# Performance work log

Measured on AMD Instinct MI355X. Metric: run time of the kernel, lower is better.

Reference implementation:

```python
import jax, jax.numpy as jnp
import numpy as np
import math

H = 32          # num_heads
D = 128         # head_dim
HID = 2048      # hidden_size
INNER = H * D   # hidden_inner_size
BLOCK = 256
NUM_LAYERS = 32
LAYER_IDX = 0


def build_slopes(n):
    def p2(m):
        start = 2 ** (-(2 ** (-(math.log2(m) - 3))))
        return [start * (start ** i) for i in range(m)]
    if math.log2(n).is_integer():
        s = p2(n)
    else:
        c = 2 ** math.floor(math.log2(n))
        s = p2(c) + p2(2 * c)[0::2][: n - c]
    s = np.asarray(s, dtype=np.float32)
    s = s * (1.0 - LAYER_IDX / (NUM_LAYERS - 1) + 1e-5)
    return jnp.asarray(s)  # [H]


def lightning_attention(q, k, v, slope, kv0, block):
    # q,k,v: [h,n,d]; slope: [h]; kv0: [h,d,e]
    h, n, d = q.shape
    nb = n // block
    arr = jnp.arange(1, block + 1, dtype=jnp.float32)            # [m]
    s = slope[:, None, None]                                      # [h,1,1]
    q_decay = jnp.exp(-s * arr[None, :, None])                    # [h,m,1]
    k_decay = jnp.exp(-s * (block - arr)[None, :, None])          # [h,m,1]
    idx = arr[:, None] - arr[None, :]                             # [m,m]
    diag_decay = jnp.where(idx >= 0, jnp.exp(-s * idx), 0.0)      # [h,m,m]
    blk_decay = jnp.exp(-slope * block)[:, None, None]            # [h,1,1]

    qb = q.reshape(h, nb, block, d).transpose(1, 0, 2, 3)         # [nb,h,m,d]
    kb = k.reshape(h, nb, block, d).transpose(1, 0, 2, 3)
    vb = v.reshape(h, nb, block, d).transpose(1, 0, 2, 3)

    def step(kv, blk):
        qi, ki, vi = blk
        inter = jnp.einsum('hmd,hde->hme', qi * q_decay, kv)
        qk = jnp.einsum('hmd,hnd->hmn', qi, ki) * diag_decay
        intra = jnp.einsum('hmn,hne->hme', qk, vi)
        kv_new = blk_decay * kv + jnp.einsum('hmd,hme->hde', ki * k_decay, vi)
        return kv_new, inter + intra

    kv_final, out = jax.lax.scan(step, kv0, (qb, kb, vb))
    out = out.transpose(1, 0, 2, 3).reshape(h, n, d)
    return out, kv_final


def rmsnorm(x, w, eps=1e-5):
    xf = x.astype(jnp.float32)
    var = jnp.mean(xf * xf, axis=-1, keepdims=True)
    return (xf * jax.lax.rsqrt(var + eps)).astype(x.dtype) * w


def setup_inputs() -> dict:
    key = jax.random.key(0)
    ks = jax.random.split(key, 4)
    n = 4096
    return {
        'hidden_states': jax.random.normal(ks[0], (n, HID), dtype=jnp.float32),
        'positions': jnp.arange(n, dtype=jnp.int64) if jax.config.jax_enable_x64 else jnp.arange(n, dtype=jnp.int32),
        'kv_cache': jnp.zeros((H, D, D), dtype=jnp.float32),
        'W_qkv': jax.random.normal(ks[1], (HID, 3 * INNER), dtype=jnp.float32) / np.sqrt(HID),
        'W_gate': jax.random.normal(ks[2], (HID, INNER), dtype=jnp.float32) / np.sqrt(HID),
        'W_out': jax.random.normal(ks[3], (INNER, HID), dtype=jnp.float32) / np.sqrt(INNER),
        'norm_weight': jnp.ones((INNER,), dtype=jnp.float32),
    }


def reference(hidden_states, positions, kv_cache, W_qkv, W_gate, W_out, norm_weight):
    n = hidden_states.shape[0]
    slope = build_slopes(H)
    qkv = hidden_states @ W_qkv                                # [n, 3*INNER]
    act = jax.nn.silu(qkv.astype(jnp.float32)).reshape(n, H, 3 * D)
    q, k, v = jnp.split(act, 3, axis=-1)                       # [n,H,D] each
    q = q.transpose(1, 0, 2)                                   # [H,n,D]
    k = k.transpose(1, 0, 2)
    v = v.transpose(1, 0, 2)
    attn, kv_final = lightning_attention(q, k, v, slope, kv_cache.astype(jnp.float32), BLOCK)
    hidden = attn.transpose(1, 0, 2).reshape(n, INNER)          # n (h d)
    hidden = rmsnorm(hidden, norm_weight)
    gate = hidden_states @ W_gate
    hidden = jax.nn.sigmoid(gate) * hidden
    out = hidden @ W_out                                        # [n, HID]
    return out
```

## Files before the change

kernel.cpp:

```cpp
#include <hip/hip_runtime.h>
#include <hip/hip_bf16.h>
#include <cstdint>
#include <cstddef>

#define SEQ    4096
#define HEADS  32
#define HD     128
#define HIDDEN 2048
#define NINNER 4096
#define BLK    256
#define NB     16

typedef __attribute__((ext_vector_type(8))) __bf16 bf16x8;
typedef __attribute__((ext_vector_type(4))) __bf16 bf16x4;
typedef __attribute__((ext_vector_type(4))) float  f32x4;

#define MFMA16(a,b,c) __builtin_amdgcn_mfma_f32_16x16x32_bf16((a),(b),(c),0,0,0)

typedef __attribute__((address_space(1))) const unsigned int gu32;
typedef __attribute__((address_space(3))) unsigned int lu32;

__device__ __forceinline__ void gld16(void* lds, const void* g){
    __builtin_amdgcn_global_load_lds((gu32*)g, (lu32*)lds, 16, 0, 0);
}

__device__ __forceinline__ float slope_for_head(int h){
    return exp2f(-0.25f*(float)(h+1)) * 1.00001f;
}

__global__ __launch_bounds__(256)
void cast_f32_bf16(const float* __restrict__ in, __bf16* __restrict__ out, int n){
    int i = (blockIdx.x*256 + threadIdx.x)*4;
    if (i >= n) return;
    float4 v = *(const float4*)(in + i);
    bf16x4 o;
    o[0] = (__bf16)v.x; o[1] = (__bf16)v.y; o[2] = (__bf16)v.z; o[3] = (__bf16)v.w;
    *(bf16x4*)(out + i) = o;
}

__global__ __launch_bounds__(256)
void transpose_cast(const float* __restrict__ W, __bf16* __restrict__ Wt, int K, int N){
    __shared__ __align__(16) __bf16 t[64][72];
    const int tid = threadIdx.x;
    const int n0 = blockIdx.x*64, k0 = blockIdx.y*64;
    const int r = tid >> 4, c4 = tid & 15;
    #pragma unroll
    for (int i = 0; i < 4; i++){
        int k = r + i*16;
        float4 v = *(const float4*)(W + (size_t)(k0 + k)*N + n0 + c4*4);
        t[c4*4+0][k] = (__bf16)v.x;
        t[c4*4+1][k] = (__bf16)v.y;
        t[c4*4+2][k] = (__bf16)v.z;
        t[c4*4+3][k] = (__bf16)v.w;
    }
    __syncthreads();
    #pragma unroll
    for (int j = 0; j < 2; j++){
        int idx = tid + j*256;
        int n = idx >> 3, c8 = idx & 7;
        bf16x8 val = *(const bf16x8*)&t[n][c8*8];
        *(bf16x8*)(Wt + (size_t)(n0 + n)*K + k0 + c8*8) = val;
    }
}

template<int EPI>
__global__ __launch_bounds__(256,2)
void gemm_bt(const __bf16* __restrict__ A, const __bf16* __restrict__ Bt,
             float* __restrict__ Cf, __bf16* __restrict__ Cb, __bf16* __restrict__ Cb2,
             int M, int N, int K)
{
    __shared__ __align__(16) __bf16 a_lds[128*64];
    __shared__ __align__(16) __bf16 b_lds[128*64];
    const int tid  = threadIdx.x;
    const int lane = tid & 63;
    const int w    = tid >> 6;
    const int lr   = lane & 15;
    const int quad = lane >> 4;
    const int bn = blockIdx.x, bm = blockIdx.y;
    const int wm = w & 1, wn = w >> 1;

    f32x4 acc[4][4];
    #pragma unroll
    for (int i = 0; i < 4; i++)
        #pragma unroll
        for (int j = 0; j < 4; j++) acc[i][j] = (f32x4){0.f,0.f,0.f,0.f};

    const int r8 = lane >> 3;
    const int qs = (lane & 7) ^ r8;
    const __bf16* Abase = A  + (size_t)bm*128*K;
    const __bf16* Bbase = Bt + (size_t)bn*128*K;

    const int sw = lr & 7;

    for (int kb = 0; kb < K; kb += 64){
        #pragma unroll
        for (int t = 0; t < 4; t++){
            int ch = t*4 + w;
            gld16(a_lds + ch*512, Abase + (size_t)(ch*8 + r8)*K + kb + qs*8);
            gld16(b_lds + ch*512, Bbase + (size_t)(ch*8 + r8)*K + kb + qs*8);
        }
        __syncthreads();
        #pragma unroll
        for (int kk = 0; kk < 2; kk++){
            bf16x8 af[4];
            #pragma unroll
            for (int mt = 0; mt < 4; mt++)
                af[mt] = *(const bf16x8*)&a_lds[(wm*64 + mt*16 + lr)*64 + (((kk*4+quad) ^ sw)*8)];
            #pragma unroll
            for (int nt = 0; nt < 4; nt++){
                bf16x8 bfv = *(const bf16x8*)&b_lds[(wn*64 + nt*16 + lr)*64 + (((kk*4+quad) ^ sw)*8)];
                #pragma unroll
                for (int mt = 0; mt < 4; mt++)
                    acc[mt][nt] = MFMA16(af[mt], bfv, acc[mt][nt]);
            }
        }
        __syncthreads();
    }

    if constexpr (EPI == 0){
        if (bn < 96){
            const int h = bn / 3, which = bn % 3;
            __bf16* outp = Cb + (size_t)(which*HEADS + h)*SEQ*HD;
            #pragma unroll
            for (int mt = 0; mt < 4; mt++)
            #pragma unroll
            for (int nt = 0; nt < 4; nt++)
            #pragma unroll
            for (int r = 0; r < 4; r++){
                int row = bm*128 + wm*64 + mt*16 + quad*4 + r;
                int col = wn*64 + nt*16 + lr;
                float x = acc[mt][nt][r];
                float sv = x / (1.f + __expf(-x));
                outp[(size_t)row*HD + col] = (__bf16)sv;
            }
        } else {
            const int col0 = (bn - 96)*128;
            #pragma unroll
            for (int mt = 0; mt < 4; mt++)
            #pragma unroll
            for (int nt = 0; nt < 4; nt++)
            #pragma unroll
            for (int r = 0; r < 4; r++){
                int row = bm*128 + wm*64 + mt*16 + quad*4 + r;
                int col = col0 + wn*64 + nt*16 + lr;
                float x = acc[mt][nt][r];
                Cb2[(size_t)row*NINNER + col] = (__bf16)(1.f/(1.f + __expf(-x)));
            }
        }
    } else {
        #pragma unroll
        for (int mt = 0; mt < 4; mt++)
        #pragma unroll
        for (int nt = 0; nt < 4; nt++)
        #pragma unroll
        for (int r = 0; r < 4; r++){
            int row = bm*128 + wm*64 + mt*16 + quad*4 + r;
            int col = bn*128 + wn*64 + nt*16 + lr;
            Cf[(size_t)row*N + col] = acc[mt][nt][r];
        }
    }
}

__global__ __launch_bounds__(256)
void prep_T(const __bf16* __restrict__ kbuf, const __bf16* __restrict__ vbuf,
            __bf16* __restrict__ kT, __bf16* __restrict__ vT)
{
    __shared__ __align__(16) __bf16 t[128][136];
    const int tid = threadIdx.x;
    const int pb = blockIdx.x, h = blockIdx.y;
    const float s = slope_for_head(h);
    const int locbase = (pb & 1)*128;
    for (int pass = 0; pass < 2; pass++){
        const __bf16* src = pass ? vbuf : kbuf;
        __bf16* dst = pass ? vT : kT;
        __syncthreads();
        #pragma unroll
        for (int i = 0; i < 8; i++){
            int idx = tid + i*256;
            int row = idx >> 4, c = idx & 15;
            bf16x8 val = *(const bf16x8*)(src + (size_t)(h*SEQ + pb*128 + row)*HD + c*8);
            if (pass == 0){
                float dec = __expf(-s*(float)(255 - (locbase + row)));
                #pragma unroll
                for (int j = 0; j < 8; j++) val[j] = (__bf16)((float)val[j]*dec);
            }
            #pragma unroll
            for (int j = 0; j < 8; j++) t[c*8 + j][row] = val[j];
        }
        __syncthreads();
        #pragma unroll
        for (int i = 0; i < 8; i++){
            int idx = tid + i*256;
            int d = idx >> 4, c = idx & 15;
            bf16x8 val = *(const bf16x8*)&t[d][c*8];
            *(bf16x8*)(dst + (size_t)(h*HD + d)*SEQ + pb*128 + c*8) = val;
        }
    }
}

__global__ __launch_bounds__(256,2)
void pass_a(const __bf16* __restrict__ vT, const __bf16* __restrict__ kT,
            float* __restrict__ kvbT)
{
    __shared__ __align__(16) __bf16 a_lds[128*64];
    __shared__ __align__(16) __bf16 b_lds[128*64];
    const int b = blockIdx.x, h = blockIdx.y;
    const int tid = threadIdx.x, lane = tid & 63, w = tid >> 6;
    const int lr = lane & 15, quad = lane >> 4;
    const int wm = w & 1, wn = w >> 1;

    f32x4 acc[4][4];
    #pragma unroll
    for (int i = 0; i < 4; i++)
        #pragma unroll
        for (int j = 0; j < 4; j++) acc[i][j] = (f32x4){0.f,0.f,0.f,0.f};

    const int r8 = lane >> 3;
    const int qs = (lane & 7) ^ r8;
    const int sw = lr & 7;
    const __bf16* Abase = vT + (size_t)h*HD*SEQ + (size_t)b*BLK;
    const __bf16* Bbase = kT + (size_t)h*HD*SEQ + (size_t)b*BLK;

    for (int kb = 0; kb < BLK; kb += 64){
        #pragma unroll
        for (int t = 0; t < 4; t++){
            int ch = t*4 + w;
            gld16(a_lds + ch*512, Abase + (size_t)(ch*8 + r8)*SEQ + kb + qs*8);
            gld16(b_lds + ch*512, Bbase + (size_t)(ch*8 + r8)*SEQ + kb + qs*8);
        }
        __syncthreads();
        #pragma unroll
        for (int kk = 0; kk < 2; kk++){
            bf16x8 af[4];
            #pragma unroll
            for (int mt = 0; mt < 4; mt++)
                af[mt] = *(const bf16x8*)&a_lds[(wm*64 + mt*16 + lr)*64 + (((kk*4+quad) ^ sw)*8)];
            #pragma unroll
            for (int nt = 0; nt < 4; nt++){
                bf16x8 bfv = *(const bf16x8*)&b_lds[(wn*64 + nt*16 + lr)*64 + (((kk*4+quad) ^ sw)*8)];
                #pragma unroll
                for (int mt = 0; mt < 4; mt++)
                    acc[mt][nt] = MFMA16(af[mt], bfv, acc[mt][nt]);
            }
        }
        __syncthreads();
    }
    float* outp = kvbT + (size_t)(h*NB + b)*HD*HD;
    #pragma unroll
    for (int mt = 0; mt < 4; mt++)
    #pragma unroll
    for (int nt = 0; nt < 4; nt++)
    #pragma unroll
    for (int r = 0; r < 4; r++){
        int row = wm*64 + mt*16 + quad*4 + r;
        int col = wn*64 + nt*16 + lr;
        outp[(size_t)row*HD + col] = acc[mt][nt][r];
    }
}

__global__ __launch_bounds__(256)
void scan_kv(const float* __restrict__ kvbT, const float* __restrict__ kv0,
             __bf16* __restrict__ kvsT)
{
    const int chunk = blockIdx.x;
    const int h = blockIdx.y;
    const int t = threadIdx.x;
    const float s = slope_for_head(h);
    const float lam = __expf(-s*(float)BLK);
    const int le0 = chunk*2048;
    float st[8];
    #pragma unroll
    for (int j = 0; j < 8; j++){
        int le = le0 + t + 256*j;
        int e = le >> 7, d = le & 127;
        st[j] = kv0[(size_t)h*HD*HD + (size_t)d*HD + e];
    }
    for (int b = 0; b < NB; b++){
        size_t base = (size_t)(h*NB + b)*HD*HD + le0;
        #pragma unroll
        for (int j = 0; j < 8; j++) kvsT[base + t + 256*j] = (__bf16)st[j];
        #pragma unroll
        for (int j = 0; j < 8; j++) st[j] = lam*st[j] + kvbT[base + t + 256*j];
    }
}

__global__ __launch_bounds__(256,2)
void pass_c(const __bf16* __restrict__ qbuf, const __bf16* __restrict__ kbuf,
            const __bf16* __restrict__ vT, const __bf16* __restrict__ kvsT,
            float* __restrict__ attn)
{
    __shared__ __align__(16) __bf16 p_lds[4][32*72];
    const int rb = blockIdx.x & 1, b = blockIdx.x >> 1, h = blockIdx.y;
    const float s = slope_for_head(h);
    const int tid = threadIdx.x, lane = tid & 63, w = tid >> 6;
    const int lr = lane & 15, quad = lane >> 4;
    const int R0 = rb*128 + w*32;

    const __bf16* qh  = qbuf + (size_t)h*SEQ*HD + (size_t)b*BLK*HD;
    const __bf16* kh  = kbuf + (size_t)h*SEQ*HD + (size_t)b*BLK*HD;
    const __bf16* vh  = vT   + (size_t)h*HD*SEQ + (size_t)b*BLK;
    const __bf16* kvh = kvsT + (size_t)(h*NB + b)*HD*HD;

    f32x4 acc[2][8];
    #pragma unroll
    for (int i = 0; i < 2; i++)
        #pragma unroll
        for (int j = 0; j < 8; j++) acc[i][j] = (f32x4){0.f,0.f,0.f,0.f};

    bf16x8 qf[4][2];
    #pragma unroll
    for (int ks = 0; ks < 4; ks++)
        #pragma unroll
        for (int mt = 0; mt < 2; mt++)
            qf[ks][mt] = *(const bf16x8*)(qh + (size_t)(R0 + mt*16 + lr)*HD + ks*32 + quad*8);

    float qdec[2];
    #pragma unroll
    for (int mt = 0; mt < 2; mt++)
        qdec[mt] = __expf(-s*(float)(R0 + mt*16 + lr + 1));
    #pragma unroll
    for (int ks = 0; ks < 4; ks++){
        bf16x8 saf[2];
        #pragma unroll
        for (int mt = 0; mt < 2; mt++)
            #pragma unroll
            for (int j = 0; j < 8; j++) saf[mt][j] = (__bf16)((float)qf[ks][mt][j]*qdec[mt]);
        #pragma unroll
        for (int nt = 0; nt < 8; nt++){
            bf16x8 bv = *(const bf16x8*)(kvh + (size_t)(nt*16 + lr)*HD + ks*32 + quad*8);
            #pragma unroll
            for (int mt = 0; mt < 2; mt++) acc[mt][nt] = MFMA16(saf[mt], bv, acc[mt][nt]);
        }
    }

    float colf[4];
    #pragma unroll
    for (int nt = 0; nt < 4; nt++)
        colf[nt] = __expf(-s*(float)(63 - nt*16 - lr));
    const int cmax = (R0 + 31) >> 6;
    for (int c = 0; c <= cmax; c++){
        f32x4 qk[2][4];
        #pragma unroll
        for (int i = 0; i < 2; i++)
            #pragma unroll
            for (int j = 0; j < 4; j++) qk[i][j] = (f32x4){0.f,0.f,0.f,0.f};
        #pragma unroll
        for (int ks = 0; ks < 4; ks++){
            #pragma unroll
            for (int nt = 0; nt < 4; nt++){
                bf16x8 kf = *(const bf16x8*)(kh + (size_t)(c*64 + nt*16 + lr)*HD + ks*32 + quad*8);
                #pragma unroll
                for (int mt = 0; mt < 2; mt++) qk[mt][nt] = MFMA16(qf[ks][mt], kf, qk[mt][nt]);
            }
        }
        float rowf[2][4];
        #pragma unroll
        for (int mt = 0; mt < 2; mt++)
            #pragma unroll
            for (int r = 0; r < 4; r++)
                rowf[mt][r] = __expf(-s*(float)(R0 + mt*16 + quad*4 + r - c*64 - 63));
        #pragma unroll
        for (int mt = 0; mt < 2; mt++)
        #pragma unroll
        for (int nt = 0; nt < 4; nt++)
        #pragma unroll
        for (int r = 0; r < 4; r++){
            int i  = R0 + mt*16 + quad*4 + r;
            int jj = c*64 + nt*16 + lr;
            float dv = (i >= jj) ? rowf[mt][r]*colf[nt] : 0.f;
            p_lds[w][(mt*16 + quad*4 + r)*72 + nt*16 + lr] = (__bf16)(qk[mt][nt][r]*dv);
        }
        #pragma unroll
        for (int ks2 = 0; ks2 < 2; ks2++){
            bf16x8 pf[2];
            #pragma unroll
            for (int mt = 0; mt < 2; mt++)
                pf[mt] = *(const bf16x8*)&p_lds[w][(mt*16 + lr)*72 + ks2*32 + quad*8];
            #pragma unroll
            for (int nt = 0; nt < 8; nt++){
                bf16x8 vf = *(const bf16x8*)(vh + (size_t)(nt*16 + lr)*SEQ + c*64 + ks2*32 + quad*8);
                #pragma unroll
                for (int mt = 0; mt < 2; mt++) acc[mt][nt] = MFMA16(pf[mt], vf, acc[mt][nt]);
            }
        }
    }

    #pragma unroll
    for (int mt = 0; mt < 2; mt++)
    #pragma unroll
    for (int nt = 0; nt < 8; nt++)
    #pragma unroll
    for (int r = 0; r < 4; r++){
        int pos = b*BLK + R0 + mt*16 + quad*4 + r;
        int e = nt*16 + lr;
        attn[(size_t)pos*NINNER + h*HD + e] = acc[mt][nt][r];
    }
}

__global__ __launch_bounds__(256)
void rmsgate(const float* __restrict__ attn, const __bf16* __restrict__ sg,
             const float* __restrict__ nw, __bf16* __restrict__ h2)
{
    const int row = blockIdx.x, tid = threadIdx.x;
    const float* x = attn + (size_t)row*NINNER;
    float4 xs[4];
    float ss = 0.f;
    #pragma unroll
    for (int i = 0; i < 4; i++){
        xs[i] = *(const float4*)(x + (i*256 + tid)*4);
        ss += xs[i].x*xs[i].x + xs[i].y*xs[i].y + xs[i].z*xs[i].z + xs[i].w*xs[i].w;
    }
    #pragma unroll
    for (int o = 32; o > 0; o >>= 1) ss += __shfl_down(ss, o, 64);
    __shared__ float red[4];
    const int lane = tid & 63, w = tid >> 6;
    if (lane == 0) red[w] = ss;
    __syncthreads();
    float tot = red[0] + red[1] + red[2] + red[3];
    float rs = rsqrtf(tot*(1.f/NINNER) + 1e-5f);
    #pragma unroll
    for (int i = 0; i < 4; i++){
        int idx = (i*256 + tid)*4;
        float4 wv = *(const float4*)(nw + idx);
        bf16x4 sv = *(const bf16x4*)(sg + (size_t)row*NINNER + idx);
        bf16x4 o;
        o[0] = (__bf16)((float)sv[0] * xs[i].x*rs*wv.x);
        o[1] = (__bf16)((float)sv[1] * xs[i].y*rs*wv.y);
        o[2] = (__bf16)((float)sv[2] * xs[i].z*rs*wv.z);
        o[3] = (__bf16)((float)sv[3] * xs[i].w*rs*wv.w);
        *(bf16x4*)(h2 + (size_t)row*NINNER + idx) = o;
    }
}

extern "C" void kernel_launch(void* const* d_in, const int* in_sizes, int n_in,
                              void* d_out, int out_size, void* d_ws, size_t ws_size,
                              hipStream_t stream) {
    (void)in_sizes; (void)n_in; (void)out_size; (void)ws_size;
    const float* hs    = (const float*)d_in[0];
    const float* kv0   = (const float*)d_in[2];
    const float* Wqkv  = (const float*)d_in[3];
    const float* Wgate = (const float*)d_in[4];
    const float* Wout  = (const float*)d_in[5];
    const float* nw    = (const float*)d_in[6];
    float* out = (float*)d_out;

    char* ws = (char*)d_ws;
    __bf16* WqkvT  = (__bf16*)(ws);
    __bf16* WgateT = (__bf16*)(ws + 50331648);
    float*  attn   = (float*)(ws);
    __bf16* WoutT  = (__bf16*)(ws + 67108864);
    __bf16* hsb    = (__bf16*)(ws + 83886080);
    __bf16* qkvb   = (__bf16*)(ws + 100663296);
    __bf16* qbuf   = qkvb;
    __bf16* kbuf   = qkvb + (size_t)HEADS*SEQ*HD;
    __bf16* vbuf   = qkvb + (size_t)2*HEADS*SEQ*HD;
    __bf16* h2     = qkvb;
    __bf16* kT     = (__bf16*)(ws + 201326592);
    __bf16* vT     = (__bf16*)(ws + 234881024);
    float*  kvbT   = (float*) (ws + 268435456);
    __bf16* kvsT   = (__bf16*)(ws + 301989888);
    __bf16* sgate  = (__bf16*)(ws + 318767104);

    cast_f32_bf16<<<8192, 256, 0, stream>>>(hs, hsb, SEQ*HIDDEN);
    transpose_cast<<<dim3(192, 32), 256, 0, stream>>>(Wqkv,  WqkvT,  2048, 12288);
    transpose_cast<<<dim3( 64, 32), 256, 0, stream>>>(Wgate, WgateT, 2048,  4096);
    transpose_cast<<<dim3( 32, 64), 256, 0, stream>>>(Wout,  WoutT,  4096,  2048);

    gemm_bt<0><<<dim3(128, 32), 256, 0, stream>>>(hsb, WqkvT, nullptr, qkvb, sgate, 4096, 16384, 2048);

    prep_T<<<dim3(32, 32), 256, 0, stream>>>(kbuf, vbuf, kT, vT);
    pass_a<<<dim3(16, 32), 256, 0, stream>>>(vT, kT, kvbT);
    scan_kv<<<dim3(8, 32), 256, 0, stream>>>(kvbT, kv0, kvsT);
    pass_c<<<dim3(NB*2, 32), 256, 0, stream>>>(qbuf, kbuf, vT, kvsT, attn);

    rmsgate<<<4096, 256, 0, stream>>>(attn, sgate, nw, h2);
    gemm_bt<2><<<dim3(16, 32), 256, 0, stream>>>(h2, WoutT, out, nullptr, nullptr, 4096, 2048, 4096);
}
```

Before: 776.0 us.

## Fuse prep kernels, switch GEMMs to 32x32 MFMA, fold transposes into QKV epilogue

```diff
diff --git a/kernel.cpp b/kernel.cpp
--- a/kernel.cpp
+++ b/kernel.cpp
@@ -11,11 +11,13 @@
 #define BLK    256
 #define NB     16
 
-typedef __attribute__((ext_vector_type(8))) __bf16 bf16x8;
-typedef __attribute__((ext_vector_type(4))) __bf16 bf16x4;
-typedef __attribute__((ext_vector_type(4))) float  f32x4;
+typedef __attribute__((ext_vector_type(8)))  __bf16 bf16x8;
+typedef __attribute__((ext_vector_type(4)))  __bf16 bf16x4;
+typedef __attribute__((ext_vector_type(4)))  float  f32x4;
+typedef __attribute__((ext_vector_type(16))) float  f32x16;
 
 #define MFMA16(a,b,c) __builtin_amdgcn_mfma_f32_16x16x32_bf16((a),(b),(c),0,0,0)
+#define MFMA32(a,b,c) __builtin_amdgcn_mfma_f32_32x32x16_bf16((a),(b),(c),0,0,0)
 
 typedef __attribute__((address_space(1))) const unsigned int gu32;
 typedef __attribute__((address_space(3))) unsigned int lu32;
@@ -28,21 +30,9 @@
     return exp2f(-0.25f*(float)(h+1)) * 1.00001f;
 }
 
-__global__ __launch_bounds__(256)
-void cast_f32_bf16(const float* __restrict__ in, __bf16* __restrict__ out, int n){
-    int i = (blockIdx.x*256 + threadIdx.x)*4;
-    if (i >= n) return;
-    float4 v = *(const float4*)(in + i);
-    bf16x4 o;
-    o[0] = (__bf16)v.x; o[1] = (__bf16)v.y; o[2] = (__bf16)v.z; o[3] = (__bf16)v.w;
-    *(bf16x4*)(out + i) = o;
-}
-
-__global__ __launch_bounds__(256)
-void transpose_cast(const float* __restrict__ W, __bf16* __restrict__ Wt, int K, int N){
-    __shared__ __align__(16) __bf16 t[64][72];
-    const int tid = threadIdx.x;
-    const int n0 = blockIdx.x*64, k0 = blockIdx.y*64;
+__device__ __forceinline__ void tcast_block(const float* __restrict__ W, __bf16* __restrict__ Wt,
+                                            int K, int N, int bx, int by, __bf16 (*t)[72], int tid){
+    const int n0 = bx*64, k0 = by*64;
     const int r = tid >> 4, c4 = tid & 15;
     #pragma unroll
     for (int i = 0; i < 4; i++){
@@ -63,34 +53,74 @@
     }
 }
 
+__global__ __launch_bounds__(256)
+void prep_all(const float* __restrict__ hs, __bf16* __restrict__ hsb,
+              const float* __restrict__ Wqkv, __bf16* __restrict__ WqkvT,
+              const float* __restrict__ Wgate, __bf16* __restrict__ WgateT,
+              const float* __restrict__ Wout, __bf16* __restrict__ WoutT)
+{
+    __shared__ __align__(16) __bf16 t[64][72];
+    const int tid = threadIdx.x;
+    int id = blockIdx.x;
+    if (id < 8192){
+        int i = (id*256 + tid)*4;
+        float4 v = *(const float4*)(hs + i);
+        bf16x4 o;
+        o[0] = (__bf16)v.x; o[1] = (__bf16)v.y; o[2] = (__bf16)v.z; o[3] = (__bf16)v.w;
+        *(bf16x4*)(hsb + i) = o;
+    } else if (id < 14336){
+        int j = id - 8192;
+        tcast_block(Wqkv, WqkvT, 2048, 12288, j % 192, j / 192, t, tid);
+    } else if (id < 16384){
+        int j = id - 14336;
+        tcast_block(Wgate, WgateT, 2048, 4096, j % 64, j / 64, t, tid);
+    } else {
+        int j = id - 16384;
+        tcast_block(Wout, WoutT, 4096, 2048, j % 32, j / 32, t, tid);
+    }
+}
+
 template<int EPI>
 __global__ __launch_bounds__(256,2)
-void gemm_bt(const __bf16* __restrict__ A, const __bf16* __restrict__ Bt,
-             float* __restrict__ Cf, __bf16* __restrict__ Cb, __bf16* __restrict__ Cb2,
-             int M, int N, int K)
+void gemm32(const __bf16* __restrict__ A, const __bf16* __restrict__ Bt,
+            float* __restrict__ Cf,
+            __bf16* __restrict__ qbuf, __bf16* __restrict__ kbuf,
+            __bf16* __restrict__ kT,   __bf16* __restrict__ vT,
+            __bf16* __restrict__ sgate,
+            int M, int N, int K)
 {
     __shared__ __align__(16) __bf16 a_lds[128*64];
     __shared__ __align__(16) __bf16 b_lds[128*64];
     const int tid  = threadIdx.x;
     const int lane = tid & 63;
     const int w    = tid >> 6;
-    const int lr   = lane & 15;
-    const int quad = lane >> 4;
-    const int bn = blockIdx.x, bm = blockIdx.y;
+    const int ml   = lane & 31;
+    const int half = lane >> 5;
     const int wm = w & 1, wn = w >> 1;
 
-    f32x4 acc[4][4];
-    #pragma unroll
-    for (int i = 0; i < 4; i++)
-        #pragma unroll
-        for (int j = 0; j < 4; j++) acc[i][j] = (f32x4){0.f,0.f,0.f,0.f};
+    int bm, bn;
+    if constexpr (EPI == 0){
+        int id = blockIdx.x;
+        bm = id & 31;
+        bn = (id >> 9)*16 + ((id >> 5) & 15);
+    } else {
+        bm = blockIdx.x & 31;
+        bn = blockIdx.x >> 5;
+    }
+
+    f32x16 acc[2][2];
+    #pragma unroll
+    for (int i = 0; i < 2; i++)
+        #pragma unroll
+        for (int j = 0; j < 2; j++)
+            #pragma unroll
+            for (int e = 0; e < 16; e++) acc[i][j][e] = 0.f;
 
     const int r8 = lane >> 3;
     const int qs = (lane & 7) ^ r8;
+    const int sw = ml & 7;
     const __bf16* Abase = A  + (size_t)bm*128*K;
     const __bf16* Bbase = Bt + (size_t)bn*128*K;
-
-    const int sw = lr & 7;
 
     for (int kb = 0; kb < K; kb += 64){
         #pragma unroll
@@ -101,17 +131,18 @@
         }
         __syncthreads();
         #pragma unroll
-        for (int kk = 0; kk < 2; kk++){
-            bf16x8 af[4];
-            #pragma unroll
-            for (int mt = 0; mt < 4; mt++)
-                af[mt] = *(const bf16x8*)&a_lds[(wm*64 + mt*16 + lr)*64 + (((kk*4+quad) ^ sw)*8)];
-            #pragma unroll
-            for (int nt = 0; nt < 4; nt++){
-                bf16x8 bfv = *(const bf16x8*)&b_lds[(wn*64 + nt*16 + lr)*64 + (((kk*4+quad) ^ sw)*8)];
-                #pragma unroll
-                for (int mt = 0; mt < 4; mt++)
-                    acc[mt][nt] = MFMA16(af[mt], bfv, acc[mt][nt]);
+        for (int kst = 0; kst < 4; kst++){
+            const int g = ((kst*2 + half) ^ sw)*8;
+            bf16x8 af[2];
+            #pragma unroll
+            for (int mt = 0; mt < 2; mt++)
+                af[mt] = *(const bf16x8*)&a_lds[(wm*64 + mt*32 + ml)*64 + g];
+            #pragma unroll
+            for (int nt = 0; nt < 2; nt++){
+                bf16x8 bfv = *(const bf16x8*)&b_lds[(wn*64 + nt*32 + ml)*64 + g];
+                #pragma unroll
+                for (int mt = 0; mt < 2; mt++)
+                    acc[mt][nt] = MFMA32(af[mt], bfv, acc[mt][nt]);
             }
         }
         __syncthreads();
@@ -120,80 +151,86 @@
     if constexpr (EPI == 0){
         if (bn < 96){
             const int h = bn / 3, which = bn % 3;
-            __bf16* outp = Cb + (size_t)(which*HEADS + h)*SEQ*HD;
-            #pragma unroll
-            for (int mt = 0; mt < 4; mt++)
-            #pragma unroll
-            for (int nt = 0; nt < 4; nt++)
-            #pragma unroll
-            for (int r = 0; r < 4; r++){
-                int row = bm*128 + wm*64 + mt*16 + quad*4 + r;
-                int col = wn*64 + nt*16 + lr;
-                float x = acc[mt][nt][r];
-                float sv = x / (1.f + __expf(-x));
-                outp[(size_t)row*HD + col] = (__bf16)sv;
+            const float s = slope_for_head(h);
+            if (which == 0){
+                #pragma unroll
+                for (int mt = 0; mt < 2; mt++)
+                #pragma unroll
+                for (int nt = 0; nt < 2; nt++)
+                #pragma unroll
+                for (int e = 0; e < 16; e++){
+                    int pos = bm*128 + wm*64 + mt*32 + (e&3) + 8*(e>>2) + 4*half;
+                    int d = wn*64 + nt*32 + ml;
+                    float x = acc[mt][nt][e];
+                    float sv = x / (1.f + __expf(-x));
+                    qbuf[((size_t)h*SEQ + pos)*HD + d] = (__bf16)sv;
+                }
+            } else if (which == 1){
+                const float es1 = __expf(s), es2 = es1*es1, es3 = es2*es1;
+                #pragma unroll
+                for (int mt = 0; mt < 2; mt++)
+                #pragma unroll
+                for (int nt = 0; nt < 2; nt++){
+                    const int d = wn*64 + nt*32 + ml;
+                    #pragma unroll
+                    for (int gq = 0; gq < 4; gq++){
+                        int pos0 = bm*128 + wm*64 + mt*32 + 8*gq + 4*half;
+                        float d0 = __expf(-s*(float)(255 - (pos0 & 255)));
+                        float dd[4] = {d0, d0*es1, d0*es2, d0*es3};
+                        bf16x4 pk;
+                        #pragma unroll
+                        for (int c = 0; c < 4; c++){
+                            float x = acc[mt][nt][gq*4 + c];
+                            float sv = x / (1.f + __expf(-x));
+                            kbuf[((size_t)h*SEQ + pos0 + c)*HD + d] = (__bf16)sv;
+                            pk[c] = (__bf16)(sv*dd[c]);
+                        }
+                        *(bf16x4*)(kT + ((size_t)h*HD + d)*SEQ + pos0) = pk;
+                    }
+                }
+            } else {
+                #pragma unroll
+                for (int mt = 0; mt < 2; mt++)
+                #pragma unroll
+                for (int nt = 0; nt < 2; nt++){
+                    const int d = wn*64 + nt*32 + ml;
+                    #pragma unroll
+                    for (int gq = 0; gq < 4; gq++){
+                        int pos0 = bm*128 + wm*64 + mt*32 + 8*gq + 4*half;
+                        bf16x4 pv;
+                        #pragma unroll
+                        for (int c = 0; c < 4; c++){
+                            float x = acc[mt][nt][gq*4 + c];
+                            pv[c] = (__bf16)(x / (1.f + __expf(-x)));
+                        }
+                        *(bf16x4*)(vT + ((size_t)h*HD + d)*SEQ + pos0) = pv;
+                    }
+                }
             }
         } else {
             const int col0 = (bn - 96)*128;
             #pragma unroll
-            for (int mt = 0; mt < 4; mt++)
-            #pragma unroll
-            for (int nt = 0; nt < 4; nt++)
-            #pragma unroll
-            for (int r = 0; r < 4; r++){
-                int row = bm*128 + wm*64 + mt*16 + quad*4 + r;
-                int col = col0 + wn*64 + nt*16 + lr;
-                float x = acc[mt][nt][r];
-                Cb2[(size_t)row*NINNER + col] = (__bf16)(1.f/(1.f + __expf(-x)));
+            for (int mt = 0; mt < 2; mt++)
+            #pragma unroll
+            for (int nt = 0; nt < 2; nt++)
+            #pragma unroll
+            for (int e = 0; e < 16; e++){
+                int row = bm*128 + wm*64 + mt*32 + (e&3) + 8*(e>>2) + 4*half;
+                int col = col0 + wn*64 + nt*32 + ml;
+                float x = acc[mt][nt][e];
+                sgate[(size_t)row*NINNER + col] = (__bf16)(1.f/(1.f + __expf(-x)));
             }
         }
     } else {
         #pragma unroll
-        for (int mt = 0; mt < 4; mt++)
-        #pragma unroll
-        for (int nt = 0; nt < 4; nt++)
-        #pragma unroll
-        for (int r = 0; r < 4; r++){
-            int row = bm*128 + wm*64 + mt*16 + quad*4 + r;
-            int col = bn*128 + wn*64 + nt*16 + lr;
-            Cf[(size_t)row*N + col] = acc[mt][nt][r];
-        }
-    }
-}
-
-__global__ __launch_bounds__(256)
-void prep_T(const __bf16* __restrict__ kbuf, const __bf16* __restrict__ vbuf,
-            __bf16* __restrict__ kT, __bf16* __restrict__ vT)
-{
-    __shared__ __align__(16) __bf16 t[128][136];
-    const int tid = threadIdx.x;
-    const int pb = blockIdx.x, h = blockIdx.y;
-    const float s = slope_for_head(h);
-    const int locbase = (pb & 1)*128;
-    for (int pass = 0; pass < 2; pass++){
-        const __bf16* src = pass ? vbuf : kbuf;
-        __bf16* dst = pass ? vT : kT;
-        __syncthreads();
-        #pragma unroll
-        for (int i = 0; i < 8; i++){
-            int idx = tid + i*256;
-            int row = idx >> 4, c = idx & 15;
-            bf16x8 val = *(const bf16x8*)(src + (size_t)(h*SEQ + pb*128 + row)*HD + c*8);
-            if (pass == 0){
-                float dec = __expf(-s*(float)(255 - (locbase + row)));
-                #pragma unroll
-                for (int j = 0; j < 8; j++) val[j] = (__bf16)((float)val[j]*dec);
-            }
-            #pragma unroll
-            for (int j = 0; j < 8; j++) t[c*8 + j][row] = val[j];
-        }
-        __syncthreads();
-        #pragma unroll
-        for (int i = 0; i < 8; i++){
-            int idx = tid + i*256;
-            int d = idx >> 4, c = idx & 15;
-            bf16x8 val = *(const bf16x8*)&t[d][c*8];
-            *(bf16x8*)(dst + (size_t)(h*HD + d)*SEQ + pb*128 + c*8) = val;
+        for (int mt = 0; mt < 2; mt++)
+        #pragma unroll
+        for (int nt = 0; nt < 2; nt++)
+        #pragma unroll
+        for (int e = 0; e < 16; e++){
+            int row = bm*128 + wm*64 + mt*32 + (e&3) + 8*(e>>2) + 4*half;
+            int col = bn*128 + wn*64 + nt*32 + ml;
+            Cf[(size_t)row*N + col] = acc[mt][nt][e];
         }
     }
 }
@@ -268,19 +305,27 @@
     const float s = slope_for_head(h);
     const float lam = __expf(-s*(float)BLK);
     const int le0 = chunk*2048;
-    float st[8];
+    float st[8], cur[8], nxt[8];
     #pragma unroll
     for (int j = 0; j < 8; j++){
         int le = le0 + t + 256*j;
         int e = le >> 7, d = le & 127;
         st[j] = kv0[(size_t)h*HD*HD + (size_t)d*HD + e];
     }
+    size_t base0 = (size_t)(h*NB)*HD*HD + le0;
+    #pragma unroll
+    for (int j = 0; j < 8; j++) cur[j] = kvbT[base0 + t + 256*j];
     for (int b = 0; b < NB; b++){
         size_t base = (size_t)(h*NB + b)*HD*HD + le0;
         #pragma unroll
         for (int j = 0; j < 8; j++) kvsT[base + t + 256*j] = (__bf16)st[j];
-        #pragma unroll
-        for (int j = 0; j < 8; j++) st[j] = lam*st[j] + kvbT[base + t + 256*j];
+        if (b < NB-1){
+            size_t nb = base + (size_t)HD*HD;
+            #pragma unroll
+            for (int j = 0; j < 8; j++) nxt[j] = kvbT[nb + t + 256*j];
+        }
+        #pragma unroll
+        for (int j = 0; j < 8; j++){ st[j] = lam*st[j] + cur[j]; cur[j] = nxt[j]; }
     }
 }
 
@@ -453,7 +498,6 @@
     __bf16* qkvb   = (__bf16*)(ws + 100663296);
     __bf16* qbuf   = qkvb;
     __bf16* kbuf   = qkvb + (size_t)HEADS*SEQ*HD;
-    __bf16* vbuf   = qkvb + (size_t)2*HEADS*SEQ*HD;
     __bf16* h2     = qkvb;
     __bf16* kT     = (__bf16*)(ws + 201326592);
     __bf16* vT     = (__bf16*)(ws + 234881024);
@@ -461,18 +505,16 @@
     __bf16* kvsT   = (__bf16*)(ws + 301989888);
     __bf16* sgate  = (__bf16*)(ws + 318767104);
 
-    cast_f32_bf16<<<8192, 256, 0, stream>>>(hs, hsb, SEQ*HIDDEN);
-    transpose_cast<<<dim3(192, 32), 256, 0, stream>>>(Wqkv,  WqkvT,  2048, 12288);
-    transpose_cast<<<dim3( 64, 32), 256, 0, stream>>>(Wgate, WgateT, 2048,  4096);
-    transpose_cast<<<dim3( 32, 64), 256, 0, stream>>>(Wout,  WoutT,  4096,  2048);
-
-    gemm_bt<0><<<dim3(128, 32), 256, 0, stream>>>(hsb, WqkvT, nullptr, qkvb, sgate, 4096, 16384, 2048);
-
-    prep_T<<<dim3(32, 32), 256, 0, stream>>>(kbuf, vbuf, kT, vT);
+    prep_all<<<18432, 256, 0, stream>>>(hs, hsb, Wqkv, WqkvT, Wgate, WgateT, Wout, WoutT);
+
+    gemm32<0><<<4096, 256, 0, stream>>>(hsb, WqkvT, nullptr, qbuf, kbuf, kT, vT, sgate,
+                                        4096, 16384, 2048);
+
     pass_a<<<dim3(16, 32), 256, 0, stream>>>(vT, kT, kvbT);
     scan_kv<<<dim3(8, 32), 256, 0, stream>>>(kvbT, kv0, kvsT);
     pass_c<<<dim3(NB*2, 32), 256, 0, stream>>>(qbuf, kbuf, vT, kvsT, attn);
 
     rmsgate<<<4096, 256, 0, stream>>>(attn, sgate, nw, h2);
-    gemm_bt<2><<<dim3(16, 32), 256, 0, stream>>>(h2, WoutT, out, nullptr, nullptr, 4096, 2048, 4096);
-}
+    gemm32<2><<<512, 256, 0, stream>>>(h2, WoutT, out, nullptr, nullptr, nullptr, nullptr, nullptr,
+                                       4096, 2048, 4096);
+}
```

New measurement: 828.5 us. 6.8% more time.
